# Kernel tuning notes

Hardware: AMD Instinct MI355X
Metric: run time of the kernel (lower is better)

## Reference

```python
import jax, jax.numpy as jnp
import numpy as np

BN_EPS = 1e-5

def _bn(x, g, b, m, v):
    # eval-mode BatchNorm1d with running stats
    return (x - m) * jax.lax.rsqrt(v + BN_EPS) * g + b

def _gcn(h, src, dst, norm, W, b, N):
    # PyG GCNConv: out[dst] += norm * (h @ W)[src]; then add bias
    msg = (h @ W)[src] * norm[:, None]
    return jax.ops.segment_sum(msg, dst, num_segments=N) + b

def setup_inputs() -> dict:
    key = jax.random.key(0)
    ks = jax.random.split(key, 24)
    N, E, F = 300000, 3000000, 25
    d = {}
    d['x'] = jax.random.normal(ks[0], (N, F), jnp.float32)
    d['edge_index'] = jax.random.randint(ks[1], (2, E), 0, N, dtype=jnp.int64)
    def lin(k, i, o):
        return jax.random.normal(k, (i, o), jnp.float32) / np.float32(np.sqrt(i))
    # ffn1: Linear(25,100) -> BN(100) -> ReLU -> Dropout -> Linear(100,25) -> BN(25) -> Dropout
    d['W1'] = lin(ks[2], 25, 100); d['b1'] = jnp.zeros((100,), jnp.float32)
    d['g1'] = jnp.ones((100,), jnp.float32); d['beta1'] = jnp.zeros((100,), jnp.float32)
    d['m1'] = jnp.zeros((100,), jnp.float32); d['v1'] = jnp.ones((100,), jnp.float32)
    d['W2'] = lin(ks[3], 100, 25); d['b2'] = jnp.zeros((25,), jnp.float32)
    d['g2'] = jnp.ones((25,), jnp.float32); d['beta2'] = jnp.zeros((25,), jnp.float32)
    d['m2'] = jnp.zeros((25,), jnp.float32); d['v2'] = jnp.ones((25,), jnp.float32)
    # GCN layers actually used in forward
    d['Wc1'] = lin(ks[4], 25, 25); d['bc1'] = jnp.zeros((25,), jnp.float32)
    d['Wc2'] = lin(ks[5], 25, 16); d['bc2'] = jnp.zeros((16,), jnp.float32)
    d['Wc3'] = lin(ks[6], 16, 16); d['bc3'] = jnp.zeros((16,), jnp.float32)
    d['Wc4'] = lin(ks[7], 16, 8);  d['bc4'] = jnp.zeros((8,), jnp.float32)
    d['Wc5'] = lin(ks[8], 8, 4);   d['bc5'] = jnp.zeros((4,), jnp.float32)
    # fc: reshape yields 1200 cols (source's Linear(4800,4) is a bug; use 1200)
    d['Wfc'] = lin(ks[9], 1200, 4); d['bfc'] = jnp.zeros((4,), jnp.float32)
    return d

def reference(x, edge_index, W1, b1, g1, beta1, m1, v1, W2, b2, g2, beta2, m2, v2,
              Wc1, bc1, Wc2, bc2, Wc3, bc3, Wc4, bc4, Wc5, bc5, Wfc, bfc):
    N = x.shape[0]
    # add self-loops and compute symmetric normalization once (shared graph)
    loops = jnp.arange(N, dtype=edge_index.dtype)
    src = jnp.concatenate([edge_index[0], loops])
    dst = jnp.concatenate([edge_index[1], loops])
    deg = jax.ops.segment_sum(jnp.ones_like(dst, jnp.float32), dst, num_segments=N)
    dinv = jnp.where(deg > 0, jax.lax.rsqrt(deg), 0.0)
    norm = dinv[src] * dinv[dst]
    # ffn1 (eval mode: dropout is identity)
    h = _bn(x @ W1 + b1, g1, beta1, m1, v1)
    h = jax.nn.relu(h)
    h = _bn(h @ W2 + b2, g2, beta2, m2, v2)
    # stacked GCN layers
    h = jax.nn.relu(_gcn(h, src, dst, norm, Wc1, bc1, N))
    h = jax.nn.relu(_gcn(h, src, dst, norm, Wc2, bc2, N))
    h = jax.nn.relu(_gcn(h, src, dst, norm, Wc3, bc3, N))
    h = jax.nn.relu(_gcn(h, src, dst, norm, Wc4, bc4, N))
    h = jax.nn.relu(_gcn(h, src, dst, norm, Wc5, bc5, N))
    h = h.reshape(-1, 300 * 4)  # [N/300, 1200]
    return h @ Wfc + bfc
```

## Files before the change

### kernel.cpp

```cpp
#include <hip/hip_runtime.h>

#define BN_EPS 1e-5f
#define ELLW 48
#define BSH2 11
#define NPB 2048
#define MAXBK 160
#define BCAP2 26624

__global__ void k_detect(const unsigned int* __restrict__ ei, int* __restrict__ flag) {
    int t = threadIdx.x;
    unsigned int v = ei[2 * t + 1];
    unsigned long long mask = __ballot(v != 0);
    if (t == 0) flag[0] = (mask == 0ULL) ? 1 : 0;
}

__global__ __launch_bounds__(256) void k_part(
    const int* __restrict__ ei, const int* __restrict__ flag,
    int* __restrict__ gcnt, int* __restrict__ bdata, int E)
{
    __shared__ int hist[MAXBK];
    __shared__ int cur[MAXBK];
    __shared__ int gbase[MAXBK];
    __shared__ int locstart[MAXBK + 1];
    __shared__ int sc[256];
    __shared__ int stage[1024];

    int t = threadIdx.x;
    int blockBase = blockIdx.x * 1024;
    int blockCnt = E - blockBase; if (blockCnt > 1024) blockCnt = 1024; if (blockCnt < 0) blockCnt = 0;

    for (int i = t; i < MAXBK; i += 256) hist[i] = 0;
    __syncthreads();

    bool w64 = (flag[0] != 0);
    int e = blockBase + t * 4;
    int s[4], d[4];
    int cnt = 0;
    if (e < E) {
        cnt = E - e; if (cnt > 4) cnt = 4;
        if (cnt == 4) {
            if (w64) {
                const int4* ps = (const int4*)(ei + (size_t)2 * e);
                int4 a = ps[0], b = ps[1];
                s[0] = a.x; s[1] = a.z; s[2] = b.x; s[3] = b.z;
                const int4* pd = (const int4*)(ei + (size_t)2 * ((size_t)E + e));
                int4 c = pd[0], f = pd[1];
                d[0] = c.x; d[1] = c.z; d[2] = f.x; d[3] = f.z;
            } else {
                int4 a = *(const int4*)(ei + e);
                s[0] = a.x; s[1] = a.y; s[2] = a.z; s[3] = a.w;
                int4 c = *(const int4*)(ei + (size_t)E + e);
                d[0] = c.x; d[1] = c.y; d[2] = c.z; d[3] = c.w;
            }
        } else {
            for (int i = 0; i < cnt; ++i) {
                if (w64) { s[i] = ei[(size_t)2 * (e + i)]; d[i] = ei[(size_t)2 * ((size_t)E + e + i)]; }
                else     { s[i] = ei[e + i];               d[i] = ei[(size_t)E + e + i]; }
            }
        }
    }
    int bk[4], pk[4];
    for (int i = 0; i < cnt; ++i) {
        bk[i] = d[i] >> BSH2;
        pk[i] = (s[i] << BSH2) | (d[i] & (NPB - 1));
        atomicAdd(&hist[bk[i]], 1);
    }
    __syncthreads();

    sc[t] = (t < MAXBK) ? hist[t] : 0;
    __syncthreads();
    for (int off = 1; off < 256; off <<= 1) {
        int x = (t >= off) ? sc[t - off] : 0;
        __syncthreads();
        sc[t] += x;
        __syncthreads();
    }
    if (t < MAXBK) {
        locstart[t] = sc[t] - hist[t];
        cur[t] = sc[t] - hist[t];
        if (hist[t] > 0) gbase[t] = atomicAdd(&gcnt[t], hist[t]);
    }
    if (t == 255) locstart[MAXBK] = sc[MAXBK - 1];
    __syncthreads();

    for (int i = 0; i < cnt; ++i) {
        int p = atomicAdd(&cur[bk[i]], 1);
        stage[p] = pk[i];
    }
    __syncthreads();

    for (int sIdx = t; sIdx < blockCnt; sIdx += 256) {
        int lo = 0, hi = MAXBK;
        while (hi - lo > 1) {
            int mid = (lo + hi) >> 1;
            if (locstart[mid] <= sIdx) lo = mid; else hi = mid;
        }
        int g = gbase[lo] + (sIdx - locstart[lo]);
        if (g < BCAP2) bdata[(size_t)lo * BCAP2 + g] = stage[sIdx];
    }
}

__global__ __launch_bounds__(256) void k_ell2(
    const int* __restrict__ gcnt, const int* __restrict__ bdata,
    int* __restrict__ ell, float* __restrict__ dinv, int N)
{
    __shared__ int lcnt[NPB];
    int b = blockIdx.x;
    int t = threadIdx.x;
    for (int i = t; i < NPB; i += 256) lcnt[i] = 0;
    __syncthreads();
    int base = b << BSH2;
    int cnt = min(gcnt[b], BCAP2);
    const int* __restrict__ bd = bdata + (size_t)b * BCAP2;
    for (int i = t; i < cnt; i += 256) {
        int v = bd[i];
        int dl = v & (NPB - 1);
        int src = v >> BSH2;
        int pos = atomicAdd(&lcnt[dl], 1);
        if (pos < ELLW - 4)
            ell[(size_t)(base + dl) * ELLW + 4 + pos] = src;
    }
    __syncthreads();
    for (int i = t; i < NPB; i += 256) {
        int n = base + i;
        if (n < N) {
            int c = lcnt[i];
            ell[(size_t)n * ELLW] = c;
            dinv[n] = 1.0f / sqrtf((float)(c + 1));
        }
    }
}

__global__ __launch_bounds__(256) void k_ffn(
    const float* __restrict__ x,
    const float* __restrict__ W1, const float* __restrict__ b1,
    const float* __restrict__ g1, const float* __restrict__ be1,
    const float* __restrict__ m1, const float* __restrict__ v1,
    const float* __restrict__ W2, const float* __restrict__ b2,
    const float* __restrict__ g2, const float* __restrict__ be2,
    const float* __restrict__ m2, const float* __restrict__ v2,
    const float* __restrict__ Wc1,
    const float* __restrict__ dinv,
    float* __restrict__ T, int N)
{
    __shared__ float sW1c[4 * 25 * 28];
    __shared__ float sW2p[100 * 28];
    __shared__ float sWcp[25 * 32];
    __shared__ float sB1[100], sS1[100];
    __shared__ float sB2[32], sS2[32];
    int t = threadIdx.x;
    if (t < 100) {
        float s = g1[t] * rsqrtf(v1[t] + BN_EPS);
        sS1[t] = s;
        sB1[t] = (b1[t] - m1[t]) * s + be1[t];
    }
    if (t >= 128 && t < 153) {
        int u = t - 128;
        float s = g2[u] * rsqrtf(v2[u] + BN_EPS);
        sS2[u] = s;
        sB2[u] = (b2[u] - m2[u]) * s + be2[u];
    }
    __syncthreads();
    for (int q = t; q < 2500; q += 256) {
        int j = q / 100, k = q % 100;
        int kc = k / 25, kk = k % 25;
        sW1c[(kc * 25 + j) * 28 + kk] = W1[q] * sS1[k];
    }
    for (int q = t; q < 2500; q += 256) {
        int k = q / 25, j2 = q % 25;
        sW2p[k * 28 + j2] = W2[q] * sS2[j2];
    }
    for (int q = t; q < 800; q += 256) {
        int k = q >> 5, j = q & 31;
        sWcp[q] = (j < 25) ? Wc1[k * 25 + j] : 0.0f;
    }
    __syncthreads();

    int g = t >> 2;
    int l = t & 3;
    int n = blockIdx.x * 64 + g;
    if (n >= N) return;

    float xi[25];
#pragma unroll
    for (int j = 0; j < 25; ++j) xi[j] = x[(size_t)n * 25 + j];

    float hm[25];
#pragma unroll
    for (int kk = 0; kk < 25; ++kk) hm[kk] = sB1[l * 25 + kk];
#pragma unroll
    for (int j = 0; j < 25; ++j) {
        float xv = xi[j];
        const float* __restrict__ wr = &sW1c[(l * 25 + j) * 28];
#pragma unroll
        for (int kk = 0; kk < 25; ++kk) hm[kk] += xv * wr[kk];
    }

    float h0[25];
#pragma unroll
    for (int j2 = 0; j2 < 25; ++j2) h0[j2] = 0.0f;
#pragma unroll
    for (int kk = 0; kk < 25; ++kk) {
        float r = fmaxf(hm[kk], 0.0f);
        const float* __restrict__ w2r = &sW2p[(l * 25 + kk) * 28];
#pragma unroll
        for (int j2 = 0; j2 < 25; ++j2) h0[j2] += r * w2r[j2];
    }
#pragma unroll
    for (int j2 = 0; j2 < 25; ++j2) {
        h0[j2] += __shfl_xor(h0[j2], 1);
        h0[j2] += __shfl_xor(h0[j2], 2);
        h0[j2] += sB2[j2];
    }

    float dv = dinv[n];
    float o[8];
#pragma unroll
    for (int jj = 0; jj < 8; ++jj) o[jj] = 0.0f;
#pragma unroll
    for (int k = 0; k < 25; ++k) {
        float hv = h0[k];
        const float* __restrict__ wr = &sWcp[k * 32 + l * 8];
#pragma unroll
        for (int jj = 0; jj < 8; ++jj) o[jj] += hv * wr[jj];
    }
    float4* T4 = (float4*)(T + (size_t)n * 32 + l * 8);
    T4[0] = make_float4(dv * o[0], dv * o[1], dv * o[2], dv * o[3]);
    T4[1] = make_float4(dv * o[4], dv * o[5], dv * o[6], dv * o[7]);
}

template <int DI, int SI, int DO, int LPN>
__global__ __launch_bounds__(256) void k_layer(
    const int* __restrict__ ell,
    const float* __restrict__ dinv, const float* __restrict__ bias,
    const float* __restrict__ W,
    const float* __restrict__ Tin, float* __restrict__ Tout, int N)
{
    constexpr int SI4 = SI / 4;
    constexpr int DO4 = DO / 4;
    constexpr int PAD = LPN * 4;
    __shared__ float sW[DI * DO];
    __shared__ float sB[PAD];
    int t = threadIdx.x;
    for (int i = t; i < DI * DO; i += 256) sW[i] = W[i];
    for (int i = t; i < PAD; i += 256) sB[i] = (i < DI) ? bias[i] : 0.0f;
    __syncthreads();

    int g = t / LPN;
    int j = t % LPN;
    int n = blockIdx.x * (256 / LPN) + g;
    int nc = (n < N) ? n : (N - 1);
    const int* __restrict__ row = ell + (size_t)nc * ELLW;
    int dg = min(row[0], ELLW - 4);
    if (n >= N) dg = 0;
    float dv = dinv[nc];
    const float4* __restrict__ T4 = (const float4*)Tin;

    float4 a0 = T4[(size_t)nc * SI4 + j];
    float4 a1 = make_float4(0.f, 0.f, 0.f, 0.f);
    float4 a2 = a1, a3 = a1;
    const int4* __restrict__ rowv = (const int4*)(row + 4);
    int k = 0;
    for (; k + 3 < dg; k += 4) {
        int4 s4 = rowv[k >> 2];
        float4 v0 = T4[(size_t)s4.x * SI4 + j];
        float4 v1 = T4[(size_t)s4.y * SI4 + j];
        float4 v2 = T4[(size_t)s4.z * SI4 + j];
        float4 v3 = T4[(size_t)s4.w * SI4 + j];
        a0.x += v0.x; a0.y += v0.y; a0.z += v0.z; a0.w += v0.w;
        a1.x += v1.x; a1.y += v1.y; a1.z += v1.z; a1.w += v1.w;
        a2.x += v2.x; a2.y += v2.y; a2.z += v2.z; a2.w += v2.w;
        a3.x += v3.x; a3.y += v3.y; a3.z += v3.z; a3.w += v3.w;
    }
    for (; k < dg; ++k) {
        float4 v = T4[(size_t)row[4 + k] * SI4 + j];
        a0.x += v.x; a0.y += v.y; a0.z += v.z; a0.w += v.w;
    }
    float ar[4];
    ar[0] = fmaxf(dv * (a0.x + a1.x + a2.x + a3.x) + sB[4 * j + 0], 0.0f);
    ar[1] = fmaxf(dv * (a0.y + a1.y + a2.y + a3.y) + sB[4 * j + 1], 0.0f);
    ar[2] = fmaxf(dv * (a0.z + a1.z + a2.z + a3.z) + sB[4 * j + 2], 0.0f);
    ar[3] = fmaxf(dv * (a0.w + a1.w + a2.w + a3.w) + sB[4 * j + 3], 0.0f);

    int lane = t & 63;
    int base = lane - j;
    int jo = (j < DO4) ? j : 0;
    const float4* __restrict__ sW4 = (const float4*)sW;
    float4 o = make_float4(0.f, 0.f, 0.f, 0.f);
#pragma unroll
    for (int k2 = 0; k2 < DI; ++k2) {
        float av = __shfl(ar[k2 & 3], base + (k2 >> 2));
        float4 w = sW4[k2 * DO4 + jo];
        o.x += av * w.x; o.y += av * w.y; o.z += av * w.z; o.w += av * w.w;
    }
    if (n < N && j < DO4)
        ((float4*)Tout)[(size_t)n * DO4 + j] =
            make_float4(dv * o.x, dv * o.y, dv * o.z, dv * o.w);
}

__global__ __launch_bounds__(256) void k_final(
    const int* __restrict__ ell,
    const float* __restrict__ dinv, const float* __restrict__ bias,
    const float* __restrict__ Tin, float* __restrict__ Tout, int N)
{
    int n = blockIdx.x * 256 + threadIdx.x;
    if (n >= N) return;
    const int* __restrict__ row = ell + (size_t)n * ELLW;
    int dg = min(row[0], ELLW - 4);
    float dv = dinv[n];
    const float4* __restrict__ T4 = (const float4*)Tin;

    float4 a0 = T4[n];
    float4 a1 = make_float4(0.f, 0.f, 0.f, 0.f);
    float4 a2 = a1, a3 = a1;
    const int4* __restrict__ rowv = (const int4*)(row + 4);
    int k = 0;
    for (; k + 3 < dg; k += 4) {
        int4 s4 = rowv[k >> 2];
        float4 v0 = T4[s4.x], v1 = T4[s4.y], v2 = T4[s4.z], v3 = T4[s4.w];
        a0.x += v0.x; a0.y += v0.y; a0.z += v0.z; a0.w += v0.w;
        a1.x += v1.x; a1.y += v1.y; a1.z += v1.z; a1.w += v1.w;
        a2.x += v2.x; a2.y += v2.y; a2.z += v2.z; a2.w += v2.w;
        a3.x += v3.x; a3.y += v3.y; a3.z += v3.z; a3.w += v3.w;
    }
    for (; k < dg; ++k) {
        float4 v = T4[row[4 + k]];
        a0.x += v.x; a0.y += v.y; a0.z += v.z; a0.w += v.w;
    }
    float4 b = *(const float4*)bias;
    ((float4*)Tout)[n] = make_float4(
        fmaxf(dv * (a0.x + a1.x + a2.x + a3.x) + b.x, 0.0f),
        fmaxf(dv * (a0.y + a1.y + a2.y + a3.y) + b.y, 0.0f),
        fmaxf(dv * (a0.z + a1.z + a2.z + a3.z) + b.z, 0.0f),
        fmaxf(dv * (a0.w + a1.w + a2.w + a3.w) + b.w, 0.0f));
}

__global__ __launch_bounds__(256) void k_fc(
    const float* __restrict__ H, const float* __restrict__ Wfc,
    const float* __restrict__ bfc, float* __restrict__ out)
{
    int r = blockIdx.x;
    int t = threadIdx.x;
    float p0 = 0.f, p1 = 0.f, p2 = 0.f, p3 = 0.f;
    for (int k = t; k < 1200; k += 256) {
        float h = H[(size_t)r * 1200 + k];
        p0 += h * Wfc[k * 4 + 0];
        p1 += h * Wfc[k * 4 + 1];
        p2 += h * Wfc[k * 4 + 2];
        p3 += h * Wfc[k * 4 + 3];
    }
#pragma unroll
    for (int off = 32; off > 0; off >>= 1) {
        p0 += __shfl_down(p0, off);
        p1 += __shfl_down(p1, off);
        p2 += __shfl_down(p2, off);
        p3 += __shfl_down(p3, off);
    }
    __shared__ float red[4][4];
    int w = t >> 6, lane = t & 63;
    if (lane == 0) { red[w][0] = p0; red[w][1] = p1; red[w][2] = p2; red[w][3] = p3; }
    __syncthreads();
    if (t < 4) {
        float s = red[0][t] + red[1][t] + red[2][t] + red[3][t];
        out[r * 4 + t] = s + bfc[t];
    }
}

extern "C" void kernel_launch(void* const* d_in, const int* in_sizes, int n_in,
                              void* d_out, int out_size, void* d_ws, size_t ws_size,
                              hipStream_t stream) {
    const float* x   = (const float*)d_in[0];
    const int*   ei  = (const int*)d_in[1];
    const float* W1  = (const float*)d_in[2];
    const float* b1  = (const float*)d_in[3];
    const float* g1  = (const float*)d_in[4];
    const float* be1 = (const float*)d_in[5];
    const float* m1  = (const float*)d_in[6];
    const float* v1  = (const float*)d_in[7];
    const float* W2  = (const float*)d_in[8];
    const float* b2  = (const float*)d_in[9];
    const float* g2  = (const float*)d_in[10];
    const float* be2 = (const float*)d_in[11];
    const float* m2  = (const float*)d_in[12];
    const float* v2  = (const float*)d_in[13];
    const float* Wc1 = (const float*)d_in[14];
    const float* bc1 = (const float*)d_in[15];
    const float* Wc2 = (const float*)d_in[16];
    const float* bc2 = (const float*)d_in[17];
    const float* Wc3 = (const float*)d_in[18];
    const float* bc3 = (const float*)d_in[19];
    const float* Wc4 = (const float*)d_in[20];
    const float* bc4 = (const float*)d_in[21];
    const float* Wc5 = (const float*)d_in[22];
    const float* bc5 = (const float*)d_in[23];
    const float* Wfc = (const float*)d_in[24];
    const float* bfc = (const float*)d_in[25];

    const int N = in_sizes[0] / 25;
    const int E = in_sizes[1] / 2;
    const int NBUCK = (N + NPB - 1) >> BSH2;

    char* ws = (char*)d_ws;
    size_t off = 0;
    auto alloc = [&](size_t bytes) { size_t o = off; off += (bytes + 255) & ~(size_t)255; return o; };
    size_t o_flag = alloc(256);
    size_t o_gcnt = alloc((size_t)MAXBK * 4);
    size_t o_dinv = alloc((size_t)N * 4);
    size_t o_ell  = alloc((size_t)N * ELLW * 4);
    size_t o_A = alloc((size_t)N * 32 * 4);
    size_t o_B = alloc((size_t)N * 16 * 4);
    (void)alloc(4096);

    int*   flag = (int*)(ws + o_flag);
    int*   gcnt = (int*)(ws + o_gcnt);
    float* dinv = (float*)(ws + o_dinv);
    int*   ell  = (int*)(ws + o_ell);
    float* A = (float*)(ws + o_A);
    float* B_ = (float*)(ws + o_B);
    int*   bdata = (int*)A;

    const int B = 256;
    int gN = (N + B - 1) / B;
    int gF = (N + 63) / 64;
    int gP = (E + 1023) / 1024;

    k_detect<<<1, 64, 0, stream>>>((const unsigned int*)ei, flag);
    hipMemsetAsync(gcnt, 0, (size_t)MAXBK * 4, stream);
    k_part<<<gP, B, 0, stream>>>(ei, flag, gcnt, bdata, E);
    k_ell2<<<NBUCK, B, 0, stream>>>(gcnt, bdata, ell, dinv, N);

    k_ffn<<<gF, B, 0, stream>>>(x, W1, b1, g1, be1, m1, v1, W2, b2, g2, be2, m2, v2,
                                Wc1, dinv, A, N);
    k_layer<25, 32, 16, 8><<<(N * 8 + B - 1) / B, B, 0, stream>>>(ell, dinv, bc1, Wc2, A, B_, N);
    k_layer<16, 16, 16, 4><<<(N * 4 + B - 1) / B, B, 0, stream>>>(ell, dinv, bc2, Wc3, B_, A, N);
    k_layer<16, 16, 8, 4><<<(N * 4 + B - 1) / B, B, 0, stream>>>(ell, dinv, bc3, Wc4, A, B_, N);
    k_layer<8, 8, 4, 2><<<(N * 2 + B - 1) / B, B, 0, stream>>>(ell, dinv, bc4, Wc5, B_, A, N);
    k_final<<<gN, B, 0, stream>>>(ell, dinv, bc5, A, B_, N);
    k_fc<<<1000, B, 0, stream>>>(B_, Wfc, bfc, (float*)d_out);
}
```

Before: 505.1 us.

## Fuse FFN with edge partition in one launch, defer dinv scaling to layer one

The FFN kernel no longer needs dinv, so it is merged with the edge-partition kernel into a single launch where some blocks run the FFN and the rest bucket edges. The FFN now handles two nodes per 4-thread group, reusing each shared-memory weight read. To drop the dinv dependency, the first GCN layer scales each gathered neighbour row and the self row by dinv, which adds a scalar gather per edge. The bucket scratch buffer moves to B_ so it does not overlap the FFN output in A.

```diff
diff --git a/kernel.cpp b/kernel.cpp
--- a/kernel.cpp
+++ b/kernel.cpp
@@ -14,89 +14,217 @@
     if (t == 0) flag[0] = (mask == 0ULL) ? 1 : 0;
 }
 
-__global__ __launch_bounds__(256) void k_part(
+struct FfnS {
+    float sW1c[4 * 25 * 28];
+    float sW2p[100 * 28];
+    float sWcp[25 * 32];
+    float sB1[100], sS1[100];
+    float sB2[32], sS2[32];
+};
+struct PartS {
+    int hist[MAXBK];
+    int cur[MAXBK];
+    int gbase[MAXBK];
+    int locstart[MAXBK + 1];
+    int sc[256];
+    int stage[1024];
+};
+
+__global__ __launch_bounds__(256) void k_ffnpart(
+    const float* __restrict__ x,
+    const float* __restrict__ W1, const float* __restrict__ b1,
+    const float* __restrict__ g1, const float* __restrict__ be1,
+    const float* __restrict__ m1, const float* __restrict__ v1,
+    const float* __restrict__ W2, const float* __restrict__ b2,
+    const float* __restrict__ g2, const float* __restrict__ be2,
+    const float* __restrict__ m2, const float* __restrict__ v2,
+    const float* __restrict__ Wc1,
+    float* __restrict__ T,
     const int* __restrict__ ei, const int* __restrict__ flag,
-    int* __restrict__ gcnt, int* __restrict__ bdata, int E)
+    int* __restrict__ gcnt, int* __restrict__ bdata,
+    int nFfn, int N, int E)
 {
-    __shared__ int hist[MAXBK];
-    __shared__ int cur[MAXBK];
-    __shared__ int gbase[MAXBK];
-    __shared__ int locstart[MAXBK + 1];
-    __shared__ int sc[256];
-    __shared__ int stage[1024];
-
+    __shared__ char smem_raw[sizeof(FfnS) > sizeof(PartS) ? sizeof(FfnS) : sizeof(PartS)];
     int t = threadIdx.x;
-    int blockBase = blockIdx.x * 1024;
-    int blockCnt = E - blockBase; if (blockCnt > 1024) blockCnt = 1024; if (blockCnt < 0) blockCnt = 0;
-
-    for (int i = t; i < MAXBK; i += 256) hist[i] = 0;
-    __syncthreads();
-
-    bool w64 = (flag[0] != 0);
-    int e = blockBase + t * 4;
-    int s[4], d[4];
-    int cnt = 0;
-    if (e < E) {
-        cnt = E - e; if (cnt > 4) cnt = 4;
-        if (cnt == 4) {
-            if (w64) {
-                const int4* ps = (const int4*)(ei + (size_t)2 * e);
-                int4 a = ps[0], b = ps[1];
-                s[0] = a.x; s[1] = a.z; s[2] = b.x; s[3] = b.z;
-                const int4* pd = (const int4*)(ei + (size_t)2 * ((size_t)E + e));
-                int4 c = pd[0], f = pd[1];
-                d[0] = c.x; d[1] = c.z; d[2] = f.x; d[3] = f.z;
+
+    if ((int)blockIdx.x < nFfn) {
+        FfnS& S = *reinterpret_cast<FfnS*>(smem_raw);
+        if (t < 100) {
+            float s = g1[t] * rsqrtf(v1[t] + BN_EPS);
+            S.sS1[t] = s;
+            S.sB1[t] = (b1[t] - m1[t]) * s + be1[t];
+        }
+        if (t >= 128 && t < 153) {
+            int u = t - 128;
+            float s = g2[u] * rsqrtf(v2[u] + BN_EPS);
+            S.sS2[u] = s;
+            S.sB2[u] = (b2[u] - m2[u]) * s + be2[u];
+        }
+        __syncthreads();
+        for (int q = t; q < 2500; q += 256) {
+            int j = q / 100, k = q % 100;
+            int kc = k / 25, kk = k % 25;
+            S.sW1c[(kc * 25 + j) * 28 + kk] = W1[q] * S.sS1[k];
+        }
+        for (int q = t; q < 2500; q += 256) {
+            int k = q / 25, j2 = q % 25;
+            S.sW2p[k * 28 + j2] = W2[q] * S.sS2[j2];
+        }
+        for (int q = t; q < 800; q += 256) {
+            int k = q >> 5, j = q & 31;
+            S.sWcp[q] = (j < 25) ? Wc1[k * 25 + j] : 0.0f;
+        }
+        __syncthreads();
+
+        int g = t >> 2;
+        int l = t & 3;
+        int n0 = ((int)blockIdx.x * 64 + g) * 2;
+        if (n0 >= N) return;
+        bool two = (n0 + 1 < N);
+        int nB = two ? n0 + 1 : n0;
+
+        float xiA[25], xiB[25];
+#pragma unroll
+        for (int j = 0; j < 25; ++j) xiA[j] = x[(size_t)n0 * 25 + j];
+#pragma unroll
+        for (int j = 0; j < 25; ++j) xiB[j] = x[(size_t)nB * 25 + j];
+
+        float hmA[25], hmB[25];
+#pragma unroll
+        for (int kk = 0; kk < 25; ++kk) { hmA[kk] = S.sB1[l * 25 + kk]; hmB[kk] = hmA[kk]; }
+#pragma unroll
+        for (int j = 0; j < 25; ++j) {
+            float xa = xiA[j], xb = xiB[j];
+            const float* __restrict__ wr = &S.sW1c[(l * 25 + j) * 28];
+#pragma unroll
+            for (int kk = 0; kk < 25; ++kk) {
+                float w = wr[kk];
+                hmA[kk] += xa * w;
+                hmB[kk] += xb * w;
+            }
+        }
+
+        float hA[25], hB[25];
+#pragma unroll
+        for (int j2 = 0; j2 < 25; ++j2) { hA[j2] = 0.0f; hB[j2] = 0.0f; }
+#pragma unroll
+        for (int kk = 0; kk < 25; ++kk) {
+            float ra = fmaxf(hmA[kk], 0.0f);
+            float rb = fmaxf(hmB[kk], 0.0f);
+            const float* __restrict__ w2r = &S.sW2p[(l * 25 + kk) * 28];
+#pragma unroll
+            for (int j2 = 0; j2 < 25; ++j2) {
+                float w = w2r[j2];
+                hA[j2] += ra * w;
+                hB[j2] += rb * w;
+            }
+        }
+#pragma unroll
+        for (int j2 = 0; j2 < 25; ++j2) {
+            hA[j2] += __shfl_xor(hA[j2], 1);
+            hA[j2] += __shfl_xor(hA[j2], 2);
+            hA[j2] += S.sB2[j2];
+            hB[j2] += __shfl_xor(hB[j2], 1);
+            hB[j2] += __shfl_xor(hB[j2], 2);
+            hB[j2] += S.sB2[j2];
+        }
+
+        float oA[8], oB[8];
+#pragma unroll
+        for (int jj = 0; jj < 8; ++jj) { oA[jj] = 0.0f; oB[jj] = 0.0f; }
+#pragma unroll
+        for (int k = 0; k < 25; ++k) {
+            float ha = hA[k], hb = hB[k];
+            const float* __restrict__ wr = &S.sWcp[k * 32 + l * 8];
+#pragma unroll
+            for (int jj = 0; jj < 8; ++jj) {
+                float w = wr[jj];
+                oA[jj] += ha * w;
+                oB[jj] += hb * w;
+            }
+        }
+        float4* TA = (float4*)(T + (size_t)n0 * 32 + l * 8);
+        TA[0] = make_float4(oA[0], oA[1], oA[2], oA[3]);
+        TA[1] = make_float4(oA[4], oA[5], oA[6], oA[7]);
+        if (two) {
+            float4* TB = (float4*)(T + (size_t)(n0 + 1) * 32 + l * 8);
+            TB[0] = make_float4(oB[0], oB[1], oB[2], oB[3]);
+            TB[1] = make_float4(oB[4], oB[5], oB[6], oB[7]);
+        }
+    } else {
+        PartS& S = *reinterpret_cast<PartS*>(smem_raw);
+        int blockBase = ((int)blockIdx.x - nFfn) * 1024;
+        int blockCnt = E - blockBase; if (blockCnt > 1024) blockCnt = 1024; if (blockCnt < 0) blockCnt = 0;
+
+        for (int i = t; i < MAXBK; i += 256) S.hist[i] = 0;
+        __syncthreads();
+
+        bool w64 = (flag[0] != 0);
+        int e = blockBase + t * 4;
+        int s[4], d[4];
+        int cnt = 0;
+        if (e < E) {
+            cnt = E - e; if (cnt > 4) cnt = 4;
+            if (cnt == 4) {
+                if (w64) {
+                    const int4* ps = (const int4*)(ei + (size_t)2 * e);
+                    int4 a = ps[0], b = ps[1];
+                    s[0] = a.x; s[1] = a.z; s[2] = b.x; s[3] = b.z;
+                    const int4* pd = (const int4*)(ei + (size_t)2 * ((size_t)E + e));
+                    int4 c = pd[0], f = pd[1];
+                    d[0] = c.x; d[1] = c.z; d[2] = f.x; d[3] = f.z;
+                } else {
+                    int4 a = *(const int4*)(ei + e);
+                    s[0] = a.x; s[1] = a.y; s[2] = a.z; s[3] = a.w;
+                    int4 c = *(const int4*)(ei + (size_t)E + e);
+                    d[0] = c.x; d[1] = c.y; d[2] = c.z; d[3] = c.w;
+                }
             } else {
-                int4 a = *(const int4*)(ei + e);
-                s[0] = a.x; s[1] = a.y; s[2] = a.z; s[3] = a.w;
-                int4 c = *(const int4*)(ei + (size_t)E + e);
-                d[0] = c.x; d[1] = c.y; d[2] = c.z; d[3] = c.w;
+                for (int i = 0; i < cnt; ++i) {
+                    if (w64) { s[i] = ei[(size_t)2 * (e + i)]; d[i] = ei[(size_t)2 * ((size_t)E + e + i)]; }
+                    else     { s[i] = ei[e + i];               d[i] = ei[(size_t)E + e + i]; }
+                }
             }
-        } else {
-            for (int i = 0; i < cnt; ++i) {
-                if (w64) { s[i] = ei[(size_t)2 * (e + i)]; d[i] = ei[(size_t)2 * ((size_t)E + e + i)]; }
-                else     { s[i] = ei[e + i];               d[i] = ei[(size_t)E + e + i]; }
+        }
+        int bk[4], pk[4];
+        for (int i = 0; i < cnt; ++i) {
+            bk[i] = d[i] >> BSH2;
+            pk[i] = (s[i] << BSH2) | (d[i] & (NPB - 1));
+            atomicAdd(&S.hist[bk[i]], 1);
+        }
+        __syncthreads();
+
+        S.sc[t] = (t < MAXBK) ? S.hist[t] : 0;
+        __syncthreads();
+        for (int off = 1; off < 256; off <<= 1) {
+            int xv = (t >= off) ? S.sc[t - off] : 0;
+            __syncthreads();
+            S.sc[t] += xv;
+            __syncthreads();
+        }
+        if (t < MAXBK) {
+            S.locstart[t] = S.sc[t] - S.hist[t];
+            S.cur[t] = S.sc[t] - S.hist[t];
+            if (S.hist[t] > 0) S.gbase[t] = atomicAdd(&gcnt[t], S.hist[t]);
+        }
+        if (t == 255) S.locstart[MAXBK] = S.sc[MAXBK - 1];
+        __syncthreads();
+
+        for (int i = 0; i < cnt; ++i) {
+            int p = atomicAdd(&S.cur[bk[i]], 1);
+            S.stage[p] = pk[i];
+        }
+        __syncthreads();
+
+        for (int sIdx = t; sIdx < blockCnt; sIdx += 256) {
+            int lo = 0, hi = MAXBK;
+            while (hi - lo > 1) {
+                int mid = (lo + hi) >> 1;
+                if (S.locstart[mid] <= sIdx) lo = mid; else hi = mid;
             }
-        }
-    }
-    int bk[4], pk[4];
-    for (int i = 0; i < cnt; ++i) {
-        bk[i] = d[i] >> BSH2;
-        pk[i] = (s[i] << BSH2) | (d[i] & (NPB - 1));
-        atomicAdd(&hist[bk[i]], 1);
-    }
-    __syncthreads();
-
-    sc[t] = (t < MAXBK) ? hist[t] : 0;
-    __syncthreads();
-    for (int off = 1; off < 256; off <<= 1) {
-        int x = (t >= off) ? sc[t - off] : 0;
-        __syncthreads();
-        sc[t] += x;
-        __syncthreads();
-    }
-    if (t < MAXBK) {
-        locstart[t] = sc[t] - hist[t];
-        cur[t] = sc[t] - hist[t];
-        if (hist[t] > 0) gbase[t] = atomicAdd(&gcnt[t], hist[t]);
-    }
-    if (t == 255) locstart[MAXBK] = sc[MAXBK - 1];
-    __syncthreads();
-
-    for (int i = 0; i < cnt; ++i) {
-        int p = atomicAdd(&cur[bk[i]], 1);
-        stage[p] = pk[i];
-    }
-    __syncthreads();
-
-    for (int sIdx = t; sIdx < blockCnt; sIdx += 256) {
-        int lo = 0, hi = MAXBK;
-        while (hi - lo > 1) {
-            int mid = (lo + hi) >> 1;
-            if (locstart[mid] <= sIdx) lo = mid; else hi = mid;
-        }
-        int g = gbase[lo] + (sIdx - locstart[lo]);
-        if (g < BCAP2) bdata[(size_t)lo * BCAP2 + g] = stage[sIdx];
+            int gp = S.gbase[lo] + (sIdx - S.locstart[lo]);
+            if (gp < BCAP2) bdata[(size_t)lo * BCAP2 + gp] = S.stage[sIdx];
+        }
     }
 }
 
@@ -131,105 +259,7 @@
     }
 }
 
-__global__ __launch_bounds__(256) void k_ffn(
-    const float* __restrict__ x,
-    const float* __restrict__ W1, const float* __restrict__ b1,
-    const float* __restrict__ g1, const float* __restrict__ be1,
-    const float* __restrict__ m1, const float* __restrict__ v1,
-    const float* __restrict__ W2, const float* __restrict__ b2,
-    const float* __restrict__ g2, const float* __restrict__ be2,
-    const float* __restrict__ m2, const float* __restrict__ v2,
-    const float* __restrict__ Wc1,
-    const float* __restrict__ dinv,
-    float* __restrict__ T, int N)
-{
-    __shared__ float sW1c[4 * 25 * 28];
-    __shared__ float sW2p[100 * 28];
-    __shared__ float sWcp[25 * 32];
-    __shared__ float sB1[100], sS1[100];
-    __shared__ float sB2[32], sS2[32];
-    int t = threadIdx.x;
-    if (t < 100) {
-        float s = g1[t] * rsqrtf(v1[t] + BN_EPS);
-        sS1[t] = s;
-        sB1[t] = (b1[t] - m1[t]) * s + be1[t];
-    }
-    if (t >= 128 && t < 153) {
-        int u = t - 128;
-        float s = g2[u] * rsqrtf(v2[u] + BN_EPS);
-        sS2[u] = s;
-        sB2[u] = (b2[u] - m2[u]) * s + be2[u];
-    }
-    __syncthreads();
-    for (int q = t; q < 2500; q += 256) {
-        int j = q / 100, k = q % 100;
-        int kc = k / 25, kk = k % 25;
-        sW1c[(kc * 25 + j) * 28 + kk] = W1[q] * sS1[k];
-    }
-    for (int q = t; q < 2500; q += 256) {
-        int k = q / 25, j2 = q % 25;
-        sW2p[k * 28 + j2] = W2[q] * sS2[j2];
-    }
-    for (int q = t; q < 800; q += 256) {
-        int k = q >> 5, j = q & 31;
-        sWcp[q] = (j < 25) ? Wc1[k * 25 + j] : 0.0f;
-    }
-    __syncthreads();
-
-    int g = t >> 2;
-    int l = t & 3;
-    int n = blockIdx.x * 64 + g;
-    if (n >= N) return;
-
-    float xi[25];
-#pragma unroll
-    for (int j = 0; j < 25; ++j) xi[j] = x[(size_t)n * 25 + j];
-
-    float hm[25];
-#pragma unroll
-    for (int kk = 0; kk < 25; ++kk) hm[kk] = sB1[l * 25 + kk];
-#pragma unroll
-    for (int j = 0; j < 25; ++j) {
-        float xv = xi[j];
-        const float* __restrict__ wr = &sW1c[(l * 25 + j) * 28];
-#pragma unroll
-        for (int kk = 0; kk < 25; ++kk) hm[kk] += xv * wr[kk];
-    }
-
-    float h0[25];
-#pragma unroll
-    for (int j2 = 0; j2 < 25; ++j2) h0[j2] = 0.0f;
-#pragma unroll
-    for (int kk = 0; kk < 25; ++kk) {
-        float r = fmaxf(hm[kk], 0.0f);
-        const float* __restrict__ w2r = &sW2p[(l * 25 + kk) * 28];
-#pragma unroll
-        for (int j2 = 0; j2 < 25; ++j2) h0[j2] += r * w2r[j2];
-    }
-#pragma unroll
-    for (int j2 = 0; j2 < 25; ++j2) {
-        h0[j2] += __shfl_xor(h0[j2], 1);
-        h0[j2] += __shfl_xor(h0[j2], 2);
-        h0[j2] += sB2[j2];
-    }
-
-    float dv = dinv[n];
-    float o[8];
-#pragma unroll
-    for (int jj = 0; jj < 8; ++jj) o[jj] = 0.0f;
-#pragma unroll
-    for (int k = 0; k < 25; ++k) {
-        float hv = h0[k];
-        const float* __restrict__ wr = &sWcp[k * 32 + l * 8];
-#pragma unroll
-        for (int jj = 0; jj < 8; ++jj) o[jj] += hv * wr[jj];
-    }
-    float4* T4 = (float4*)(T + (size_t)n * 32 + l * 8);
-    T4[0] = make_float4(dv * o[0], dv * o[1], dv * o[2], dv * o[3]);
-    T4[1] = make_float4(dv * o[4], dv * o[5], dv * o[6], dv * o[7]);
-}
-
-template <int DI, int SI, int DO, int LPN>
+template <int DI, int SI, int DO, int LPN, bool SDV>
 __global__ __launch_bounds__(256) void k_layer(
     const int* __restrict__ ell,
     const float* __restrict__ dinv, const float* __restrict__ bias,
@@ -257,6 +287,7 @@
     const float4* __restrict__ T4 = (const float4*)Tin;
 
     float4 a0 = T4[(size_t)nc * SI4 + j];
+    if (SDV) { a0.x *= dv; a0.y *= dv; a0.z *= dv; a0.w *= dv; }
     float4 a1 = make_float4(0.f, 0.f, 0.f, 0.f);
     float4 a2 = a1, a3 = a1;
     const int4* __restrict__ rowv = (const int4*)(row + 4);
@@ -267,14 +298,24 @@
         float4 v1 = T4[(size_t)s4.y * SI4 + j];
         float4 v2 = T4[(size_t)s4.z * SI4 + j];
         float4 v3 = T4[(size_t)s4.w * SI4 + j];
-        a0.x += v0.x; a0.y += v0.y; a0.z += v0.z; a0.w += v0.w;
-        a1.x += v1.x; a1.y += v1.y; a1.z += v1.z; a1.w += v1.w;
-        a2.x += v2.x; a2.y += v2.y; a2.z += v2.z; a2.w += v2.w;
-        a3.x += v3.x; a3.y += v3.y; a3.z += v3.z; a3.w += v3.w;
+        if (SDV) {
+            float d0 = dinv[s4.x], d1 = dinv[s4.y], d2 = dinv[s4.z], d3 = dinv[s4.w];
+            a0.x += d0 * v0.x; a0.y += d0 * v0.y; a0.z += d0 * v0.z; a0.w += d0 * v0.w;
+            a1.x += d1 * v1.x; a1.y += d1 * v1.y; a1.z += d1 * v1.z; a1.w += d1 * v1.w;
+            a2.x += d2 * v2.x; a2.y += d2 * v2.y; a2.z += d2 * v2.z; a2.w += d2 * v2.w;
+            a3.x += d3 * v3.x; a3.y += d3 * v3.y; a3.z += d3 * v3.z; a3.w += d3 * v3.w;
+        } else {
+            a0.x += v0.x; a0.y += v0.y; a0.z += v0.z; a0.w += v0.w;
+            a1.x += v1.x; a1.y += v1.y; a1.z += v1.z; a1.w += v1.w;
+            a2.x += v2.x; a2.y += v2.y; a2.z += v2.z; a2.w += v2.w;
+            a3.x += v3.x; a3.y += v3.y; a3.z += v3.z; a3.w += v3.w;
+        }
     }
     for (; k < dg; ++k) {
-        float4 v = T4[(size_t)row[4 + k] * SI4 + j];
-        a0.x += v.x; a0.y += v.y; a0.z += v.z; a0.w += v.w;
+        int sidx = row[4 + k];
+        float4 v = T4[(size_t)sidx * SI4 + j];
+        float dd = SDV ? dinv[sidx] : 1.0f;
+        a0.x += dd * v.x; a0.y += dd * v.y; a0.z += dd * v.z; a0.w += dd * v.w;
     }
     float ar[4];
     ar[0] = fmaxf(dv * (a0.x + a1.x + a2.x + a3.x) + sB[4 * j + 0], 0.0f);
@@ -417,24 +458,23 @@
     int*   ell  = (int*)(ws + o_ell);
     float* A = (float*)(ws + o_A);
     float* B_ = (float*)(ws + o_B);
-    int*   bdata = (int*)A;
+    int*   bdata = (int*)B_;
 
     const int B = 256;
     int gN = (N + B - 1) / B;
-    int gF = (N + 63) / 64;
+    int gF = (N + 127) / 128;
     int gP = (E + 1023) / 1024;
 
     k_detect<<<1, 64, 0, stream>>>((const unsigned int*)ei, flag);
     hipMemsetAsync(gcnt, 0, (size_t)MAXBK * 4, stream);
-    k_part<<<gP, B, 0, stream>>>(ei, flag, gcnt, bdata, E);
+    k_ffnpart<<<gF + gP, B, 0, stream>>>(x, W1, b1, g1, be1, m1, v1, W2, b2, g2, be2, m2, v2,
+                                         Wc1, A, ei, flag, gcnt, bdata, gF, N, E);
     k_ell2<<<NBUCK, B, 0, stream>>>(gcnt, bdata, ell, dinv, N);
 
-    k_ffn<<<gF, B, 0, stream>>>(x, W1, b1, g1, be1, m1, v1, W2, b2, g2, be2, m2, v2,
-                                Wc1, dinv, A, N);
-    k_layer<25, 32, 16, 8><<<(N * 8 + B - 1) / B, B, 0, stream>>>(ell, dinv, bc1, Wc2, A, B_, N);
-    k_layer<16, 16, 16, 4><<<(N * 4 + B - 1) / B, B, 0, stream>>>(ell, dinv, bc2, Wc3, B_, A, N);
-    k_layer<16, 16, 8, 4><<<(N * 4 + B - 1) / B, B, 0, stream>>>(ell, dinv, bc3, Wc4, A, B_, N);
-    k_layer<8, 8, 4, 2><<<(N * 2 + B - 1) / B, B, 0, stream>>>(ell, dinv, bc4, Wc5, B_, A, N);
+    k_layer<25, 32, 16, 8, true><<<(N * 8 + B - 1) / B, B, 0, stream>>>(ell, dinv, bc1, Wc2, A, B_, N);
+    k_layer<16, 16, 16, 4, false><<<(N * 4 + B - 1) / B, B, 0, stream>>>(ell, dinv, bc2, Wc3, B_, A, N);
+    k_layer<16, 16, 8, 4, false><<<(N * 4 + B - 1) / B, B, 0, stream>>>(ell, dinv, bc3, Wc4, A, B_, N);
+    k_layer<8, 8, 4, 2, false><<<(N * 2 + B - 1) / B, B, 0, stream>>>(ell, dinv, bc4, Wc5, B_, A, N);
     k_final<<<gN, B, 0, stream>>>(ell, dinv, bc5, A, B_, N);
     k_fc<<<1000, B, 0, stream>>>(B_, Wfc, bfc, (float*)d_out);
 }
```

Measured after the change: 610.3 us. 1.21x slower.
